# Kernel optimization log

Hardware: AMD Instinct MI355X
Metric: run time of the kernel (lower is better)

## Reference

```python
import math
import jax, jax.numpy as jnp
import numpy as np

D_MODEL = 4096
N_HEADS = 32
N_KV_HEADS = 8
D_HEAD = D_MODEL // N_HEADS  # 128
GROUP = N_HEADS // N_KV_HEADS  # 4
ROPE = dict(rope_theta=500000.0, factor=32.0, hi_freq_factor=4.0, lo_freq_factor=1.0, original_context_length=8192)


def setup_inputs() -> dict:
    key = jax.random.key(0)
    ks = jax.random.split(key, 5)
    B, T = 1, 2048
    s = 0.02
    return {
        "resid": jax.random.normal(ks[0], (B, T, D_MODEL), jnp.float32),
        "Wq": jax.random.normal(ks[1], (D_MODEL, D_MODEL), jnp.float32) * s,
        "Wk": jax.random.normal(ks[2], (D_MODEL, N_KV_HEADS * D_HEAD), jnp.float32) * s,
        "Wv": jax.random.normal(ks[3], (D_MODEL, N_KV_HEADS * D_HEAD), jnp.float32) * s,
        "Wo": jax.random.normal(ks[4], (D_MODEL, D_MODEL), jnp.float32) * s,
    }


def _rope_cos_sin(head_dim, pos, dtype):
    # Llama3 scaled RoPE frequencies
    idx = jnp.arange(0, head_dim, 2, dtype=jnp.float32) / head_dim
    freq = (1.0 / (2.0 * math.pi)) * ROPE["rope_theta"] ** (-idx)
    factor, lo, hi = ROPE["factor"], ROPE["lo_freq_factor"], ROPE["hi_freq_factor"]
    L0 = ROPE["original_context_length"]
    freq_low, freq_high = lo / L0, hi / L0
    freq_scaled = jnp.where(freq < freq_low, freq / factor, freq)
    smooth = jnp.clip((L0 * freq - lo) / (hi - lo), 0.0, 1.0)
    freq_smooth = (1.0 - smooth) * (freq / factor) + smooth * freq
    is_mid = (freq >= freq_low) & (freq <= freq_high)
    freq = jnp.where(is_mid, freq_smooth, freq_scaled)
    phase = 2.0 * math.pi * pos.astype(jnp.float32)[:, None] * freq[None, :]  # [T, dh/2]
    emb = jnp.concatenate([phase, phase], axis=-1)  # [T, dh]
    return jnp.cos(emb).astype(dtype), jnp.sin(emb).astype(dtype)


def _rotate_half(x):
    h = x.shape[-1] // 2
    return jnp.concatenate([-x[..., h:], x[..., :h]], axis=-1)


def reference(resid, Wq, Wk, Wv, Wo):
    B, T, _ = resid.shape
    # projections + head split -> [B, H, T, dh]
    q = (resid @ Wq).reshape(B, T, N_HEADS, D_HEAD).transpose(0, 2, 1, 3)
    k = (resid @ Wk).reshape(B, T, N_KV_HEADS, D_HEAD).transpose(0, 2, 1, 3)
    v = (resid @ Wv).reshape(B, T, N_KV_HEADS, D_HEAD).transpose(0, 2, 1, 3)
    cos, sin = _rope_cos_sin(D_HEAD, jnp.arange(T), resid.dtype)  # [T, dh]
    cos = cos[None, None]  # broadcast over batch and heads
    sin = sin[None, None]
    q = q * cos + _rotate_half(q) * sin
    k = k * cos + _rotate_half(k) * sin
    # GQA scores in fp32: [B, Hkv, G, Tq, Tk]
    qg = q.reshape(B, N_KV_HEADS, GROUP, T, D_HEAD)
    att = jnp.einsum("bhgqd,bhkd->bhgqk", qg.astype(jnp.float32), k.astype(jnp.float32)) / math.sqrt(D_HEAD)
    causal = jnp.tril(jnp.ones((T, T), dtype=bool))  # k <= q
    att = jnp.where(causal[None, None, None], att, -jnp.inf)
    probs = jax.nn.softmax(att, axis=-1).astype(resid.dtype)
    ctx = jnp.einsum("bhgqk,bhkd->bhgqd", probs, v)  # [B, Hkv, G, T, dh]
    out = ctx.reshape(B, N_HEADS, T, D_HEAD).transpose(0, 2, 1, 3).reshape(B, T, D_MODEL)
    return out @ Wo
```

## Files before the change

kernel.cpp:

```cpp
#include <hip/hip_runtime.h>
#include <stdint.h>

#define T_SEQ 2048
#define DMODEL 4096
#define DQKV 6144
#define KOFF 4096
#define VOFF 5120
#define DHEAD 128
#define NHEADS 32
#define NKV 8

typedef unsigned short u16;
typedef __attribute__((ext_vector_type(8))) __bf16 bf16x8;
typedef __attribute__((ext_vector_type(4))) float f32x4;

__device__ __forceinline__ u16 f2bf(float f) {
    uint32_t u = __builtin_bit_cast(uint32_t, f);
    u += 0x7FFFu + ((u >> 16) & 1u);
    return (u16)(u >> 16);
}
__device__ __forceinline__ float bf2f(u16 b) {
    return __builtin_bit_cast(float, (uint32_t)b << 16);
}

__device__ __forceinline__ void gload_lds16(const u16* g, u16* l) {
    __builtin_amdgcn_global_load_lds((const __attribute__((address_space(1))) uint32_t*)g,
                                     (__attribute__((address_space(3))) uint32_t*)l, 16, 0, 0);
}

__global__ void cvt_kernel(const float* __restrict__ in, u16* __restrict__ out, int n4) {
    int i = blockIdx.x * blockDim.x + threadIdx.x;
    int stride = gridDim.x * blockDim.x;
    for (; i < n4; i += stride) {
        float4 v = ((const float4*)in)[i];
        ushort4 o;
        o.x = f2bf(v.x); o.y = f2bf(v.y); o.z = f2bf(v.z); o.w = f2bf(v.w);
        ((ushort4*)out)[i] = o;
    }
}

__global__ void tcvt4_kernel(const float* __restrict__ Wq, const float* __restrict__ Wk,
                             const float* __restrict__ Wv, const float* __restrict__ Wo,
                             u16* __restrict__ WqT, u16* __restrict__ WkT,
                             u16* __restrict__ WvT, u16* __restrict__ WoT) {
    __shared__ float tile[32][33];
    int bid = blockIdx.x;
    const float* in; u16* out; int C, s;
    if (bid < 16384)      { in = Wq; out = WqT; C = DMODEL; s = bid; }
    else if (bid < 20480) { in = Wk; out = WkT; C = 1024;   s = bid - 16384; }
    else if (bid < 24576) { in = Wv; out = WvT; C = 1024;   s = bid - 20480; }
    else                  { in = Wo; out = WoT; C = DMODEL; s = bid - 24576; }
    int ntx = C / 32;
    int c0 = (s % ntx) * 32, r0 = (s / ntx) * 32;
    int tx = threadIdx.x, ty = threadIdx.y;
#pragma unroll
    for (int i = 0; i < 32; i += 8)
        tile[ty + i][tx] = in[(size_t)(r0 + ty + i) * C + c0 + tx];
    __syncthreads();
#pragma unroll
    for (int i = 0; i < 32; i += 8)
        out[(size_t)(c0 + ty + i) * DMODEL + r0 + tx] = f2bf(tile[tx][ty + i]);
}

__global__ void vtrans_kernel(const u16* __restrict__ QKV, u16* __restrict__ Vt) {
    __shared__ u16 tile[32][33];
    int t0 = blockIdx.x * 32, d0 = blockIdx.y * 32;
    int tx = threadIdx.x, ty = threadIdx.y;
#pragma unroll
    for (int i = 0; i < 32; i += 8)
        tile[ty + i][tx] = QKV[(size_t)(t0 + ty + i) * DQKV + VOFF + d0 + tx];
    __syncthreads();
#pragma unroll
    for (int i = 0; i < 32; i += 8)
        Vt[(size_t)(d0 + ty + i) * T_SEQ + t0 + tx] = tile[tx][ty + i];
}

__global__ void rope_setup(float* __restrict__ cosT, float* __restrict__ sinT) {
    int t = blockIdx.x, d = threadIdx.x;
    const float TWO_PI = 6.283185307179586f;
    float fidx = (float)d * (1.0f / 64.0f);
    float freq = (1.0f / TWO_PI) * powf(500000.0f, -fidx);
    const float factor = 32.0f, lo = 1.0f, hi = 4.0f, L0 = 8192.0f;
    float fl = lo / L0, fh = hi / L0;
    float smooth = fminf(fmaxf((L0 * freq - lo) / (hi - lo), 0.0f), 1.0f);
    float fs = (1.0f - smooth) * (freq / factor) + smooth * freq;
    float fr = (freq < fl) ? (freq / factor) : freq;
    if (freq >= fl && freq <= fh) fr = fs;
    float ang = TWO_PI * (float)t * fr;
    cosT[t * 64 + d] = cosf(ang);
    sinT[t * 64 + d] = sinf(ang);
}

__global__ void rope_all(u16* __restrict__ x, const float* __restrict__ cosT,
                         const float* __restrict__ sinT) {
    int i = blockIdx.x * blockDim.x + threadIdx.x;
    int total = T_SEQ * 40 * 64;
    if (i >= total) return;
    int d = i & 63;
    int h = (i >> 6) % 40;
    int t = i / (40 * 64);
    int col = (h < 32) ? (h * 128 + d) : (KOFF + (h - 32) * 128 + d);
    size_t base = (size_t)t * DQKV + col;
    float x0 = bf2f(x[base]), x1 = bf2f(x[base + 64]);
    float c = cosT[t * 64 + d], s = sinT[t * 64 + d];
    x[base] = f2bf(x0 * c - x1 * s);
    x[base + 64] = f2bf(x1 * c + x0 * s);
}

template<int BM, int BN, int WR, int WC, int E>
__launch_bounds__(512, 1)
__global__ void gemm8p(const u16* __restrict__ A, const u16* __restrict__ Bt,
                       void* __restrict__ Cout, int M, int N, int K, int f32out) {
    constexpr int WM = BM / WR, WN = BN / WC;
    constexpr int FM = WM / 16, FN = WN / 16;
    constexpr int FMH = FM / 2, FNH = FN / 2;
    constexpr int NCH = (BM + BN) / 64;
    constexpr int TILE = (BM + BN) * 64;
    static_assert(E * 64 <= BM, "E-region must stay within A rows (P4/P8 read B)");
    extern __shared__ u16 lds[];

    int tid = threadIdx.x;
    int lane = tid & 63, wid = tid >> 6;
    int l15 = lane & 15, lg = lane >> 4;
    int wm0 = (wid / WC) * WM, wn0 = (wid % WC) * WN;
    int m0 = blockIdx.y * BM, n0 = blockIdx.x * BN;
    int rsw = l15 & 7;
    int rl = tid >> 3, cc = tid & 7;
    int scc = cc ^ (rl & 7);
    const u16* Ag = A + (size_t)(m0 + rl) * K + scc * 8;
    const u16* Bg = Bt + (size_t)(n0 + rl) * K + scc * 8;
    int niters = K >> 7;

    f32x4 acc[FM][FN] = {};
    bf16x8 aQ0[FMH][2], aQ1[FMH][2];
    bf16x8 bQ0[FNH][2], bQ1[FNH][2];

    auto stg = [&](int buf, int t, int clo, int chi) {
#pragma unroll
        for (int c = 0; c < NCH; ++c)
            if (c >= clo && c < chi) {
                const u16* g = (c * 64 < BM) ? (Ag + (size_t)(c * 64) * K + (size_t)t * 64)
                                             : (Bg + (size_t)(c * 64 - BM) * K + (size_t)t * 64);
                gload_lds16(g, lds + buf * TILE + c * 4096 + tid * 8);
            }
    };

#define RDA(buf, qm, DST) { _Pragma("unroll") for (int mi = 0; mi < FMH; ++mi) { \
    int row = wm0 + (qm) * (WM / 2) + mi * 16 + l15; \
    _Pragma("unroll") for (int h = 0; h < 2; ++h) \
        DST[mi][h] = *(const bf16x8*)&lds[(buf) * TILE + row * 64 + (((h * 4 + lg) ^ rsw) * 8)]; } }
#define RDB(buf, qn, DST) { _Pragma("unroll") for (int ni = 0; ni < FNH; ++ni) { \
    int row = wn0 + (qn) * (WN / 2) + ni * 16 + l15; \
    _Pragma("unroll") for (int h = 0; h < 2; ++h) \
        DST[ni][h] = *(const bf16x8*)&lds[(buf) * TILE + BM * 64 + row * 64 + (((h * 4 + lg) ^ rsw) * 8)]; } }
#define MMQ(AR, BR, qm, qn) { _Pragma("unroll") for (int mi = 0; mi < FMH; ++mi) \
    _Pragma("unroll") for (int ni = 0; ni < FNH; ++ni) { \
    acc[(qm)*FMH+mi][(qn)*FNH+ni] = __builtin_amdgcn_mfma_f32_16x16x32_bf16(AR[mi][0], BR[ni][0], acc[(qm)*FMH+mi][(qn)*FNH+ni], 0, 0, 0); \
    acc[(qm)*FMH+mi][(qn)*FNH+ni] = __builtin_amdgcn_mfma_f32_16x16x32_bf16(AR[mi][1], BR[ni][1], acc[(qm)*FMH+mi][(qn)*FNH+ni], 0, 0, 0); } }
#define SB0     __builtin_amdgcn_sched_barrier(0)
#define BAR     __builtin_amdgcn_s_barrier()
#define PRIO1   __builtin_amdgcn_s_setprio(1)
#define PRIO0   __builtin_amdgcn_s_setprio(0)
#define FENCE_E asm volatile("s_waitcnt vmcnt(%0)" :: "i"(E) : "memory")
#define FENCE_0 asm volatile("s_waitcnt vmcnt(0)" ::: "memory")

    stg(0, 0, 0, NCH);
    stg(1, 1, 0, E);
    FENCE_E; SB0; BAR;
    RDA(0, 0, aQ0); RDB(0, 0, bQ0);

    for (int it = 0; it < niters; ++it) {
        int t0 = 2 * it, t1 = t0 + 1;
        bool last = (it == niters - 1);
        RDB(0, 1, bQ1);
        stg(1, t1, E, NCH);
        SB0; BAR; SB0; PRIO1; MMQ(aQ0, bQ0, 0, 0); PRIO0; BAR;
        RDA(0, 1, aQ1);
        SB0; BAR; SB0; PRIO1; MMQ(aQ0, bQ1, 0, 1); PRIO0; BAR;
        SB0; BAR; SB0; PRIO1; MMQ(aQ1, bQ1, 1, 1); PRIO0; BAR;
        if (!last) stg(0, t0 + 2, 0, E);
        SB0; BAR; SB0; PRIO1; MMQ(aQ1, bQ0, 1, 0); PRIO0;
        if (last) { FENCE_0; } else { FENCE_E; }
        SB0; BAR;
        RDA(1, 0, aQ0); RDB(1, 0, bQ0);
        RDB(1, 1, bQ1);
        if (!last) stg(0, t0 + 2, E, NCH);
        SB0; BAR; SB0; PRIO1; MMQ(aQ0, bQ0, 0, 0); PRIO0; BAR;
        RDA(1, 1, aQ1);
        SB0; BAR; SB0; PRIO1; MMQ(aQ0, bQ1, 0, 1); PRIO0; BAR;
        SB0; BAR; SB0; PRIO1; MMQ(aQ1, bQ1, 1, 1); PRIO0; BAR;
        if (!last) stg(1, t1 + 2, 0, E);
        SB0; BAR; SB0; PRIO1; MMQ(aQ1, bQ0, 1, 0); PRIO0;
        if (!last) {
            FENCE_E; SB0; BAR;
            RDA(0, 0, aQ0); RDB(0, 0, bQ0);
        }
    }
#undef RDA
#undef RDB
#undef MMQ
#undef SB0
#undef BAR
#undef PRIO1
#undef PRIO0
#undef FENCE_E
#undef FENCE_0

#pragma unroll
    for (int fm = 0; fm < FM; ++fm)
#pragma unroll
        for (int fn = 0; fn < FN; ++fn)
#pragma unroll
            for (int r = 0; r < 4; ++r) {
                int row = m0 + wm0 + fm * 16 + lg * 4 + r;
                int col = n0 + wn0 + fn * 16 + l15;
                float v = acc[fm][fn][r];
                if (f32out) ((float*)Cout)[(size_t)row * N + col] = v;
                else        ((u16*)Cout)[(size_t)row * N + col] = f2bf(v);
            }
}

__launch_bounds__(256, 3)
__global__ void attn_kernel(const u16* __restrict__ QKV, const u16* __restrict__ Vt,
                            u16* __restrict__ ctx) {
    __shared__ u16 Ks[2][64][128];
    __shared__ u16 Vs[2][128][64];
    __shared__ u16 Ones[16][64];
    __shared__ u16 Ps[4][16][72];
    int h = blockIdx.x;
    int q0 = ((int)gridDim.y - 1 - (int)blockIdx.y) * 64;
    int kvh = h >> 2;
    int tid = threadIdx.x;
    int lane = tid & 63;
    int wave = tid >> 6;
    int l15 = lane & 15, lg = lane >> 4;
    int qrow_base = q0 + wave * 16;

    {
        int idx = tid * 4;
        u16 val = (idx < 64) ? (u16)0x3F80 : (u16)0;
        u16* p = &Ones[0][0] + idx;
        p[0] = val; p[1] = val; p[2] = val; p[3] = val;
    }

    bf16x8 qf[4];
#pragma unroll
    for (int kk = 0; kk < 4; ++kk)
        qf[kk] = *(const bf16x8*)&QKV[(size_t)(qrow_base + l15) * DQKV + h * DHEAD + kk * 32 + lg * 8];

    int krow = tid >> 4, kj = tid & 15;
    int vrow = tid >> 3, vj = tid & 7;
    const u16* Kg = QKV + (size_t)krow * DQKV + KOFF + kvh * DHEAD + ((kj ^ krow) * 8);
    const u16* Vg = Vt + (size_t)(kvh * DHEAD + vrow) * T_SEQ + ((vj ^ (vrow & 7)) * 8);
    u16* Kl = &Ks[0][0][0] + tid * 8;
    u16* Vl = &Vs[0][0][0] + tid * 8;
    const int BUFK = 64 * 128;
    const int BUFV = 128 * 64;

#define STAGE(buf, kv0)                                                              \
    {                                                                                \
        _Pragma("unroll")                                                            \
        for (int p = 0; p < 4; ++p) {                                                \
            gload_lds16(Kg + (size_t)((kv0) + p * 16) * DQKV, Kl + (buf) * BUFK + p * 2048); \
            gload_lds16(Vg + (kv0) + (size_t)(p * 32) * T_SEQ, Vl + (buf) * BUFV + p * 2048); \
        }                                                                            \
    }

    f32x4 acc_o[8] = {};
    f32x4 acc_l = {0.f, 0.f, 0.f, 0.f};
    float m_run[4];
#pragma unroll
    for (int r = 0; r < 4; ++r) m_run[r] = -1e30f;

    int ntiles = (q0 >> 6) + 1;
    STAGE(0, 0);

    for (int t = 0; t < ntiles; ++t) {
        int cur = t & 1;
        __syncthreads();
        if (t + 1 < ntiles) STAGE(cur ^ 1, (t + 1) * 64);

        const u16* ksb = &Ks[cur][0][0];
        const u16* vsb = &Vs[cur][0][0];
        int kv0 = t * 64;

        f32x4 sacc[4] = {};
#pragma unroll
        for (int nt = 0; nt < 4; ++nt)
#pragma unroll
            for (int kk = 0; kk < 4; ++kk) {
                int row = nt * 16 + l15;
                int slot = (kk * 4 + lg) ^ l15;
                bf16x8 kf = *(const bf16x8*)(ksb + row * 128 + slot * 8);
                sacc[nt] = __builtin_amdgcn_mfma_f32_16x16x32_bf16(qf[kk], kf, sacc[nt], 0, 0, 0);
            }

        const float scale = 0.08838834764831845f;
        bool diag = (t == ntiles - 1);
#pragma unroll
        for (int r = 0; r < 4; ++r) {
            int qrow = qrow_base + lg * 4 + r;
            float sv[4];
            float pmax = -1e30f;
#pragma unroll
            for (int nt = 0; nt < 4; ++nt) {
                float s = sacc[nt][r] * scale;
                if (diag && (kv0 + nt * 16 + l15 > qrow)) s = -1e30f;
                sv[nt] = s;
                pmax = fmaxf(pmax, s);
            }
#pragma unroll
            for (int m = 1; m < 16; m <<= 1) pmax = fmaxf(pmax, __shfl_xor(pmax, m, 64));
            if (__any(pmax > m_run[r] + 8.0f)) {
                float mnew = fmaxf(m_run[r], pmax);
                float alpha = __expf(m_run[r] - mnew);
                m_run[r] = mnew;
#pragma unroll
                for (int dt = 0; dt < 8; ++dt) acc_o[dt][r] *= alpha;
                acc_l[r] *= alpha;
            }
#pragma unroll
            for (int nt = 0; nt < 4; ++nt)
                Ps[wave][lg * 4 + r][nt * 16 + l15] = f2bf(__expf(sv[nt] - m_run[r]));
        }

        bf16x8 pf[2];
#pragma unroll
        for (int kt = 0; kt < 2; ++kt)
            pf[kt] = *(const bf16x8*)&Ps[wave][l15][kt * 32 + lg * 8];
#pragma unroll
        for (int kt = 0; kt < 2; ++kt) {
            int oslot = (kt * 4 + lg) ^ (l15 & 7);
            bf16x8 of = *(const bf16x8*)(&Ones[0][0] + l15 * 64 + oslot * 8);
            acc_l = __builtin_amdgcn_mfma_f32_16x16x32_bf16(pf[kt], of, acc_l, 0, 0, 0);
        }
#pragma unroll
        for (int dt = 0; dt < 8; ++dt)
#pragma unroll
            for (int kt = 0; kt < 2; ++kt) {
                int vr = dt * 16 + l15;
                int slot = (kt * 4 + lg) ^ (l15 & 7);
                bf16x8 vf = *(const bf16x8*)(vsb + vr * 64 + slot * 8);
                acc_o[dt] = __builtin_amdgcn_mfma_f32_16x16x32_bf16(pf[kt], vf, acc_o[dt], 0, 0, 0);
            }
    }
#undef STAGE

#pragma unroll
    for (int r = 0; r < 4; ++r) {
        float lsum = __shfl(acc_l[r], lg * 16, 64);
        float inv = 1.0f / lsum;
#pragma unroll
        for (int dt = 0; dt < 8; ++dt) {
            int row = qrow_base + lg * 4 + r;
            int col = h * DHEAD + dt * 16 + l15;
            ctx[(size_t)row * DMODEL + col] = f2bf(acc_o[dt][r] * inv);
        }
    }
}

extern "C" void kernel_launch(void* const* d_in, const int* in_sizes, int n_in,
                              void* d_out, int out_size, void* d_ws, size_t ws_size,
                              hipStream_t stream) {
    const float* resid = (const float*)d_in[0];
    const float* Wq = (const float*)d_in[1];
    const float* Wk = (const float*)d_in[2];
    const float* Wv = (const float*)d_in[3];
    const float* Wo = (const float*)d_in[4];

    char* ws = (char*)d_ws;
    u16* Xb   = (u16*)(ws + 0);
    u16* ctx  = (u16*)(ws + 0);
    u16* WqT  = (u16*)(ws + 16777216);
    u16* WkT  = (u16*)(ws + 50331648);
    u16* WvT  = (u16*)(ws + 58720256);
    u16* WoT  = (u16*)(ws + 67108864);
    u16* QKV  = (u16*)(ws + 100663296);
    u16* Vt   = (u16*)(ws + 125829120);
    float* cosT = (float*)(ws + 130023424);
    float* sinT = (float*)(ws + 130547712);

    cvt_kernel<<<2048, 256, 0, stream>>>(resid, Xb, T_SEQ * DMODEL / 4);
    dim3 tb(32, 8);
    tcvt4_kernel<<<40960, tb, 0, stream>>>(Wq, Wk, Wv, Wo, WqT, WkT, WvT, WoT);
    rope_setup<<<T_SEQ, 64, 0, stream>>>(cosT, sinT);

    gemm8p<256, 192, 4, 2, 4><<<dim3(DQKV / 192, T_SEQ / 256), 512, (256 + 192) * 64 * 2 * 2, stream>>>(
        Xb, WqT, QKV, T_SEQ, DQKV, DMODEL, 0);

    rope_all<<<(T_SEQ * 40 * 64 + 255) / 256, 256, 0, stream>>>(QKV, cosT, sinT);

    vtrans_kernel<<<dim3(T_SEQ / 32, 1024 / 32), tb, 0, stream>>>(QKV, Vt);

    attn_kernel<<<dim3(NHEADS, T_SEQ / 64), 256, 0, stream>>>(QKV, Vt, ctx);

    gemm8p<128, 256, 2, 4, 2><<<dim3(DMODEL / 256, T_SEQ / 128), 512, (128 + 256) * 64 * 2 * 2, stream>>>(
        ctx, WoT, d_out, T_SEQ, DMODEL, DMODEL, 1);
}
```

Measured before the change: 322.1 us.

## Process 128 query rows per attention block with two row groups per wave

Doubles the query tile per attention block from 64 to 128 rows, so each wave handles two 16-row groups that share every K/V tile staged in LDS. This halves the K/V global-to-LDS traffic and the number of blocks, in exchange for more registers per thread (launch bounds lowered to 2 blocks per CU) and fewer blocks to spread the causal workload across. The causal mask now applies to the last two KV tiles.

```diff
diff --git a/kernel.cpp b/kernel.cpp
--- a/kernel.cpp
+++ b/kernel.cpp
@@ -220,7 +220,7 @@
             }
 }
 
-__launch_bounds__(256, 3)
+__launch_bounds__(256, 2)
 __global__ void attn_kernel(const u16* __restrict__ QKV, const u16* __restrict__ Vt,
                             u16* __restrict__ ctx) {
     __shared__ u16 Ks[2][64][128];
@@ -228,13 +228,13 @@
     __shared__ u16 Ones[16][64];
     __shared__ u16 Ps[4][16][72];
     int h = blockIdx.x;
-    int q0 = ((int)gridDim.y - 1 - (int)blockIdx.y) * 64;
+    int q0 = ((int)gridDim.y - 1 - (int)blockIdx.y) * 128;
     int kvh = h >> 2;
     int tid = threadIdx.x;
     int lane = tid & 63;
     int wave = tid >> 6;
     int l15 = lane & 15, lg = lane >> 4;
-    int qrow_base = q0 + wave * 16;
+    int qrow_base = q0 + wave * 32;
 
     {
         int idx = tid * 4;
@@ -243,10 +243,12 @@
         p[0] = val; p[1] = val; p[2] = val; p[3] = val;
     }
 
-    bf16x8 qf[4];
-#pragma unroll
-    for (int kk = 0; kk < 4; ++kk)
-        qf[kk] = *(const bf16x8*)&QKV[(size_t)(qrow_base + l15) * DQKV + h * DHEAD + kk * 32 + lg * 8];
+    bf16x8 qf[2][4];
+#pragma unroll
+    for (int rg = 0; rg < 2; ++rg)
+#pragma unroll
+        for (int kk = 0; kk < 4; ++kk)
+            qf[rg][kk] = *(const bf16x8*)&QKV[(size_t)(qrow_base + rg * 16 + l15) * DQKV + h * DHEAD + kk * 32 + lg * 8];
 
     int krow = tid >> 4, kj = tid & 15;
     int vrow = tid >> 3, vj = tid & 7;
@@ -266,13 +268,13 @@
         }                                                                            \
     }
 
-    f32x4 acc_o[8] = {};
-    f32x4 acc_l = {0.f, 0.f, 0.f, 0.f};
-    float m_run[4];
-#pragma unroll
-    for (int r = 0; r < 4; ++r) m_run[r] = -1e30f;
-
-    int ntiles = (q0 >> 6) + 1;
+    f32x4 acc_o0[8] = {}, acc_o1[8] = {};
+    f32x4 acc_l0 = {0.f, 0.f, 0.f, 0.f}, acc_l1 = {0.f, 0.f, 0.f, 0.f};
+    float m_run0[4], m_run1[4];
+#pragma unroll
+    for (int r = 0; r < 4; ++r) { m_run0[r] = -1e30f; m_run1[r] = -1e30f; }
+
+    int ntiles = (q0 >> 6) + 2;
     STAGE(0, 0);
 
     for (int t = 0; t < ntiles; ++t) {
@@ -284,7 +286,7 @@
         const u16* vsb = &Vs[cur][0][0];
         int kv0 = t * 64;
 
-        f32x4 sacc[4] = {};
+        f32x4 sacc0[4] = {}, sacc1[4] = {};
 #pragma unroll
         for (int nt = 0; nt < 4; ++nt)
 #pragma unroll
@@ -292,69 +294,85 @@
                 int row = nt * 16 + l15;
                 int slot = (kk * 4 + lg) ^ l15;
                 bf16x8 kf = *(const bf16x8*)(ksb + row * 128 + slot * 8);
-                sacc[nt] = __builtin_amdgcn_mfma_f32_16x16x32_bf16(qf[kk], kf, sacc[nt], 0, 0, 0);
+                sacc0[nt] = __builtin_amdgcn_mfma_f32_16x16x32_bf16(qf[0][kk], kf, sacc0[nt], 0, 0, 0);
+                sacc1[nt] = __builtin_amdgcn_mfma_f32_16x16x32_bf16(qf[1][kk], kf, sacc1[nt], 0, 0, 0);
             }
 
         const float scale = 0.08838834764831845f;
-        bool diag = (t == ntiles - 1);
+        bool maskzone = (t >= ntiles - 2);
+
+#pragma unroll
+        for (int rg = 0; rg < 2; ++rg) {
+            f32x4* sacc = (rg == 0) ? sacc0 : sacc1;
+            f32x4* acc_o = (rg == 0) ? acc_o0 : acc_o1;
+            f32x4& acc_l = (rg == 0) ? acc_l0 : acc_l1;
+            float* m_run = (rg == 0) ? m_run0 : m_run1;
+            int rowb = qrow_base + rg * 16;
+
+#pragma unroll
+            for (int r = 0; r < 4; ++r) {
+                int qrow = rowb + lg * 4 + r;
+                float sv[4];
+                float pmax = -1e30f;
+#pragma unroll
+                for (int nt = 0; nt < 4; ++nt) {
+                    float s = sacc[nt][r] * scale;
+                    if (maskzone && (kv0 + nt * 16 + l15 > qrow)) s = -1e30f;
+                    sv[nt] = s;
+                    pmax = fmaxf(pmax, s);
+                }
+#pragma unroll
+                for (int m = 1; m < 16; m <<= 1) pmax = fmaxf(pmax, __shfl_xor(pmax, m, 64));
+                if (__any(pmax > m_run[r] + 8.0f)) {
+                    float mnew = fmaxf(m_run[r], pmax);
+                    float alpha = __expf(m_run[r] - mnew);
+                    m_run[r] = mnew;
+#pragma unroll
+                    for (int dt = 0; dt < 8; ++dt) acc_o[dt][r] *= alpha;
+                    acc_l[r] *= alpha;
+                }
+#pragma unroll
+                for (int nt = 0; nt < 4; ++nt)
+                    Ps[wave][lg * 4 + r][nt * 16 + l15] = f2bf(__expf(sv[nt] - m_run[r]));
+            }
+
+            bf16x8 pf[2];
+#pragma unroll
+            for (int kt = 0; kt < 2; ++kt)
+                pf[kt] = *(const bf16x8*)&Ps[wave][l15][kt * 32 + lg * 8];
+#pragma unroll
+            for (int kt = 0; kt < 2; ++kt) {
+                int oslot = (kt * 4 + lg) ^ (l15 & 7);
+                bf16x8 of = *(const bf16x8*)(&Ones[0][0] + l15 * 64 + oslot * 8);
+                acc_l = __builtin_amdgcn_mfma_f32_16x16x32_bf16(pf[kt], of, acc_l, 0, 0, 0);
+            }
+#pragma unroll
+            for (int dt = 0; dt < 8; ++dt)
+#pragma unroll
+                for (int kt = 0; kt < 2; ++kt) {
+                    int vr = dt * 16 + l15;
+                    int slot = (kt * 4 + lg) ^ (l15 & 7);
+                    bf16x8 vf = *(const bf16x8*)(vsb + vr * 64 + slot * 8);
+                    acc_o[dt] = __builtin_amdgcn_mfma_f32_16x16x32_bf16(pf[kt], vf, acc_o[dt], 0, 0, 0);
+                }
+        }
+    }
+#undef STAGE
+
+#pragma unroll
+    for (int rg = 0; rg < 2; ++rg) {
+        f32x4* acc_o = (rg == 0) ? acc_o0 : acc_o1;
+        f32x4& acc_l = (rg == 0) ? acc_l0 : acc_l1;
 #pragma unroll
         for (int r = 0; r < 4; ++r) {
-            int qrow = qrow_base + lg * 4 + r;
-            float sv[4];
-            float pmax = -1e30f;
-#pragma unroll
-            for (int nt = 0; nt < 4; ++nt) {
-                float s = sacc[nt][r] * scale;
-                if (diag && (kv0 + nt * 16 + l15 > qrow)) s = -1e30f;
-                sv[nt] = s;
-                pmax = fmaxf(pmax, s);
-            }
-#pragma unroll
-            for (int m = 1; m < 16; m <<= 1) pmax = fmaxf(pmax, __shfl_xor(pmax, m, 64));
-            if (__any(pmax > m_run[r] + 8.0f)) {
-                float mnew = fmaxf(m_run[r], pmax);
-                float alpha = __expf(m_run[r] - mnew);
-                m_run[r] = mnew;
-#pragma unroll
-                for (int dt = 0; dt < 8; ++dt) acc_o[dt][r] *= alpha;
-                acc_l[r] *= alpha;
-            }
-#pragma unroll
-            for (int nt = 0; nt < 4; ++nt)
-                Ps[wave][lg * 4 + r][nt * 16 + l15] = f2bf(__expf(sv[nt] - m_run[r]));
-        }
-
-        bf16x8 pf[2];
-#pragma unroll
-        for (int kt = 0; kt < 2; ++kt)
-            pf[kt] = *(const bf16x8*)&Ps[wave][l15][kt * 32 + lg * 8];
-#pragma unroll
-        for (int kt = 0; kt < 2; ++kt) {
-            int oslot = (kt * 4 + lg) ^ (l15 & 7);
-            bf16x8 of = *(const bf16x8*)(&Ones[0][0] + l15 * 64 + oslot * 8);
-            acc_l = __builtin_amdgcn_mfma_f32_16x16x32_bf16(pf[kt], of, acc_l, 0, 0, 0);
-        }
-#pragma unroll
-        for (int dt = 0; dt < 8; ++dt)
-#pragma unroll
-            for (int kt = 0; kt < 2; ++kt) {
-                int vr = dt * 16 + l15;
-                int slot = (kt * 4 + lg) ^ (l15 & 7);
-                bf16x8 vf = *(const bf16x8*)(vsb + vr * 64 + slot * 8);
-                acc_o[dt] = __builtin_amdgcn_mfma_f32_16x16x32_bf16(pf[kt], vf, acc_o[dt], 0, 0, 0);
-            }
-    }
-#undef STAGE
-
-#pragma unroll
-    for (int r = 0; r < 4; ++r) {
-        float lsum = __shfl(acc_l[r], lg * 16, 64);
-        float inv = 1.0f / lsum;
-#pragma unroll
-        for (int dt = 0; dt < 8; ++dt) {
-            int row = qrow_base + lg * 4 + r;
-            int col = h * DHEAD + dt * 16 + l15;
-            ctx[(size_t)row * DMODEL + col] = f2bf(acc_o[dt][r] * inv);
+            float lsum = __shfl(acc_l[r], lg * 16, 64);
+            float inv = 1.0f / lsum;
+#pragma unroll
+            for (int dt = 0; dt < 8; ++dt) {
+                int row = qrow_base + rg * 16 + lg * 4 + r;
+                int col = h * DHEAD + dt * 16 + l15;
+                ctx[(size_t)row * DMODEL + col] = f2bf(acc_o[dt][r] * inv);
+            }
         }
     }
 }
@@ -392,7 +410,7 @@
 
     vtrans_kernel<<<dim3(T_SEQ / 32, 1024 / 32), tb, 0, stream>>>(QKV, Vt);
 
-    attn_kernel<<<dim3(NHEADS, T_SEQ / 64), 256, 0, stream>>>(QKV, Vt, ctx);
+    attn_kernel<<<dim3(NHEADS, T_SEQ / 128), 256, 0, stream>>>(QKV, Vt, ctx);
 
     gemm8p<128, 256, 2, 4, 2><<<dim3(DMODEL / 256, T_SEQ / 128), 512, (128 + 256) * 64 * 2 * 2, stream>>>(
         ctx, WoT, d_out, T_SEQ, DMODEL, DMODEL, 1);
```

Measured after the change: 339.0 us. 5.2% more time.
